# Performance work log

Measured on AMD Instinct MI355X. Metric: run time of the kernel, lower is better.

Reference implementation:

```python
import jax, jax.numpy as jnp
import numpy as np

B, N, D, H, F = 16, 257, 1024, 16, 4096
HD = D // H
EPS = 1e-5
GATING_TEMP = 0.25  # gating_hyperparam for steep_sigmoid
SCALE = HD ** -0.5


def layer_norm(x, g, b):
    mu = jnp.mean(x, axis=-1, keepdims=True)
    var = jnp.mean(jnp.square(x - mu), axis=-1, keepdims=True)
    return (x - mu) * jax.lax.rsqrt(var + EPS) * g + b


def quick_gelu(x):
    return x * jax.nn.sigmoid(1.702 * x)


def setup_inputs() -> dict:
    key = jax.random.key(0)
    ks = jax.random.split(key, 24)
    s = 0.02
    inp = {
        'hidden_states': jax.random.normal(ks[0], (B, N, D), jnp.float32),
        'cached_hidden': jax.random.normal(ks[1], (B, N, D), jnp.float32),
        'cached_q': jax.random.normal(ks[2], (B, N, D), jnp.float32),
        'cached_k': jax.random.normal(ks[3], (B, N, D), jnp.float32),
        'cached_v': jax.random.normal(ks[4], (B, N, D), jnp.float32),
        'ln1_g': jnp.ones((D,), jnp.float32),
        'ln1_b': jnp.zeros((D,), jnp.float32),
        'wq': jax.random.normal(ks[5], (D, D), jnp.float32) * s,
        'bq': jnp.zeros((D,), jnp.float32),
        'wk': jax.random.normal(ks[6], (D, D), jnp.float32) * s,
        'bk': jnp.zeros((D,), jnp.float32),
        'wv': jax.random.normal(ks[7], (D, D), jnp.float32) * s,
        'bv': jnp.zeros((D,), jnp.float32),
        'wo': jax.random.normal(ks[8], (D, D), jnp.float32) * s,
        'bo': jnp.zeros((D,), jnp.float32),
        'ln2_g': jnp.ones((D,), jnp.float32),
        'ln2_b': jnp.zeros((D,), jnp.float32),
        'w1': jax.random.normal(ks[9], (D, F), jnp.float32) * s,
        'b1': jnp.zeros((F,), jnp.float32),
        'w2': jax.random.normal(ks[10], (F, D), jnp.float32) * s,
        'b2': jnp.zeros((D,), jnp.float32),
        'threshold': jnp.float32(0.5),
    }
    return inp


def reference(hidden_states, cached_hidden, cached_q, cached_k, cached_v,
              ln1_g, ln1_b, wq, bq, wk, bk, wv, bv, wo, bo,
              ln2_g, ln2_b, w1, b1, w2, b2, threshold):
    # layer_norm1 + QKV projection (layer_norm1_qkv_projection)
    h_ln = layer_norm(hidden_states, ln1_g, ln1_b)
    q = h_ln @ wq + bq
    k = h_ln @ wk + bk
    v = h_ln @ wv + bv

    # reuse module: cosine^1 similarity vs cached hidden, steep_sigmoid gating
    # against learned threshold; soft gather/scatter blend of cached states.
    num = jnp.sum(cached_hidden * hidden_states, axis=-1)           # [B,N]
    den = (jnp.linalg.norm(cached_hidden, axis=-1)
           * jnp.linalg.norm(hidden_states, axis=-1) + 1e-8)
    sim = num / den                                                 # [B,N]
    gate = jax.nn.sigmoid((sim - threshold) / GATING_TEMP)[..., None]  # [B,N,1]

    hidden = gate * cached_hidden + (1.0 - gate) * hidden_states
    q = gate * cached_q + (1.0 - gate) * q
    k = gate * cached_k + (1.0 - gate) * k
    v = gate * cached_v + (1.0 - gate) * v

    # manual bmm-softmax-bmm attention
    qh = (q * SCALE).reshape(B, N, H, HD).transpose(0, 2, 1, 3)  # [B,H,N,hd]
    kh = k.reshape(B, N, H, HD).transpose(0, 2, 1, 3)
    vh = v.reshape(B, N, H, HD).transpose(0, 2, 1, 3)
    scores = jnp.einsum('bhqd,bhkd->bhqk', qh, kh)
    probs = jax.nn.softmax(scores, axis=-1)
    attn = jnp.einsum('bhqk,bhkd->bhqd', probs, vh)
    attn = attn.transpose(0, 2, 1, 3).reshape(B, N, D)
    attn = attn @ wo + bo

    hidden = hidden + attn
    residual = hidden
    hidden = layer_norm(hidden, ln2_g, ln2_b)
    hidden = quick_gelu(hidden @ w1 + b1) @ w2 + b2
    return residual + hidden
```

## Files before the change

kernel.cpp:

```cpp
#include <hip/hip_runtime.h>
#include <hip/hip_bf16.h>
#include <stdint.h>

#define BB   16
#define SEQ  257
#define DD   1024
#define NH   16
#define HD_  64
#define FF   4096
#define MM   (BB*SEQ)
#define MPAD2 4352
#define SPAD 272
#define VPAD 288
#define SCALE_Q 0.125f

typedef __bf16 bf16x8 __attribute__((ext_vector_type(8)));
typedef float  f32x4  __attribute__((ext_vector_type(4)));
typedef unsigned short u16;

__device__ __forceinline__ u16 f2bf(float f) {
  uint32_t u = __float_as_uint(f);
  uint32_t r = (u + 0x7FFFu + ((u >> 16) & 1u)) >> 16;
  return (u16)r;
}
__device__ __forceinline__ float bf2f(u16 u) {
  return __uint_as_float(((uint32_t)u) << 16);
}
__device__ __forceinline__ void gll16(const void* g, void* l) {
  __builtin_amdgcn_global_load_lds(
      (const __attribute__((address_space(1))) void*)g,
      (__attribute__((address_space(3))) void*)l, 16, 0, 0);
}
__device__ __forceinline__ float wsum(float v) {
  #pragma unroll
  for (int o = 1; o < 64; o <<= 1) v += __shfl_xor(v, o);
  return v;
}

__global__ __launch_bounds__(256) void transpose_all(
    const float* __restrict__ wq, const float* __restrict__ wk,
    const float* __restrict__ wv, const float* __restrict__ wo,
    const float* __restrict__ w1, const float* __restrict__ w2,
    u16* __restrict__ wqkvT, u16* __restrict__ woT,
    u16* __restrict__ w1T, u16* __restrict__ w2T) {
  __shared__ float tile[64][65];
  const int bid = blockIdx.x;
  const float* src;  u16* dst;  int R, C, b;
  if (bid < 768)       { int s = bid >> 8;  b = bid & 255;
                         src = s==0?wq:(s==1?wk:wv);  dst = wqkvT + s*1024*1024;
                         R = 1024; C = 1024; }
  else if (bid < 1024) { src = wo;  dst = woT;  b = bid - 768;   R = 1024; C = 1024; }
  else if (bid < 2048) { src = w1;  dst = w1T;  b = bid - 1024;  R = 1024; C = 4096; }
  else                 { src = w2;  dst = w2T;  b = bid - 2048;  R = 4096; C = 1024; }
  const int ctiles = C >> 6;
  const int r0 = (b / ctiles) << 6, c0 = (b % ctiles) << 6;
  const int tx = threadIdx.x & 63, ty = threadIdx.x >> 6;
  #pragma unroll
  for (int it = 0; it < 16; ++it) {
    int rr = it * 4 + ty;
    tile[rr][tx] = src[(size_t)(r0 + rr) * C + c0 + tx];
  }
  __syncthreads();
  #pragma unroll
  for (int it = 0; it < 16; ++it) {
    int rr = it * 4 + ty;
    dst[(size_t)(c0 + rr) * R + r0 + tx] = f2bf(tile[tx][rr]);
  }
}

__global__ __launch_bounds__(256) void vtrans_kernel(
    const u16* __restrict__ vb, u16* __restrict__ vt) {
  __shared__ u16 tile[64][72];
  const int bh = blockIdx.x, c = blockIdx.y;
  const int tx = threadIdx.x & 63, ty = threadIdx.x >> 6;
  const u16* src = vb + (size_t)bh * SPAD * HD_;
  u16* dst = vt + (size_t)bh * HD_ * VPAD;
  #pragma unroll
  for (int it = 0; it < 16; ++it) {
    int r = it * 4 + ty;
    int nn = c * 64 + r;  int nnc = nn < SPAD ? nn : SPAD - 1;
    tile[r][tx] = src[(size_t)nnc * HD_ + tx];
  }
  __syncthreads();
  #pragma unroll
  for (int it = 0; it < 16; ++it) {
    int hd = it * 4 + ty;
    int col = c * 64 + tx;
    if (col < VPAD) dst[(size_t)hd * VPAD + col] = tile[tx][hd];
  }
}

__global__ __launch_bounds__(256) void ln1_gate_kernel(
    const float* __restrict__ h, const float* __restrict__ c,
    const float* __restrict__ g, const float* __restrict__ bta,
    const float* __restrict__ thr, u16* __restrict__ hln,
    float* __restrict__ hblend, float* __restrict__ gate) {
  int m = blockIdx.x, t = threadIdx.x, l = t & 63, w = t >> 6;
  const float4 hv = *(const float4*)(h + (size_t)m * DD + t * 4);
  const float4 cv = *(const float4*)(c + (size_t)m * DD + t * 4);
  float sh = hv.x + hv.y + hv.z + hv.w;
  float sh2 = hv.x*hv.x + hv.y*hv.y + hv.z*hv.z + hv.w*hv.w;
  float sch = hv.x*cv.x + hv.y*cv.y + hv.z*cv.z + hv.w*cv.w;
  float sc2 = cv.x*cv.x + cv.y*cv.y + cv.z*cv.z + cv.w*cv.w;
  sh = wsum(sh); sh2 = wsum(sh2); sch = wsum(sch); sc2 = wsum(sc2);
  __shared__ float red[4][4];
  if (l == 0) { red[w][0]=sh; red[w][1]=sh2; red[w][2]=sch; red[w][3]=sc2; }
  __syncthreads();
  float Sh  = red[0][0]+red[1][0]+red[2][0]+red[3][0];
  float Sh2 = red[0][1]+red[1][1]+red[2][1]+red[3][1];
  float Sch = red[0][2]+red[1][2]+red[2][2]+red[3][2];
  float Sc2 = red[0][3]+red[1][3]+red[2][3]+red[3][3];
  float mean = Sh * (1.f/DD);
  float var  = Sh2 * (1.f/DD) - mean*mean;
  float rs   = rsqrtf(var + 1e-5f);
  float sim  = Sch / (sqrtf(Sc2)*sqrtf(Sh2) + 1e-8f);
  float gv   = 1.f / (1.f + __expf(-(sim - thr[0]) * 4.0f));
  float4 gg = *(const float4*)(g + t*4);
  float4 bb = *(const float4*)(bta + t*4);
  ushort4 ob;
  ob.x = f2bf((hv.x-mean)*rs*gg.x + bb.x);
  ob.y = f2bf((hv.y-mean)*rs*gg.y + bb.y);
  ob.z = f2bf((hv.z-mean)*rs*gg.z + bb.z);
  ob.w = f2bf((hv.w-mean)*rs*gg.w + bb.w);
  *(ushort4*)(hln + (size_t)m * DD + t * 4) = ob;
  float4 hb;
  hb.x = gv*cv.x + (1.f-gv)*hv.x;  hb.y = gv*cv.y + (1.f-gv)*hv.y;
  hb.z = gv*cv.z + (1.f-gv)*hv.z;  hb.w = gv*cv.w + (1.f-gv)*hv.w;
  *(float4*)(hblend + (size_t)m * DD + t * 4) = hb;
  if (t == 0) gate[m] = gv;
}

__global__ __launch_bounds__(256) void ln2_kernel(
    const float* __restrict__ in, const float* __restrict__ g,
    const float* __restrict__ bta, u16* __restrict__ outb) {
  int m = blockIdx.x, t = threadIdx.x, l = t & 63, w = t >> 6;
  const float4 hv = *(const float4*)(in + (size_t)m * DD + t * 4);
  float sh = hv.x + hv.y + hv.z + hv.w;
  float sh2 = hv.x*hv.x + hv.y*hv.y + hv.z*hv.z + hv.w*hv.w;
  sh = wsum(sh); sh2 = wsum(sh2);
  __shared__ float red[4][2];
  if (l == 0) { red[w][0] = sh; red[w][1] = sh2; }
  __syncthreads();
  float Sh  = red[0][0]+red[1][0]+red[2][0]+red[3][0];
  float Sh2 = red[0][1]+red[1][1]+red[2][1]+red[3][1];
  float mean = Sh * (1.f/DD);
  float rs = rsqrtf(Sh2 * (1.f/DD) - mean*mean + 1e-5f);
  float4 gg = *(const float4*)(g + t*4);
  float4 bb = *(const float4*)(bta + t*4);
  ushort4 ob;
  ob.x = f2bf((hv.x-mean)*rs*gg.x + bb.x);
  ob.y = f2bf((hv.y-mean)*rs*gg.y + bb.y);
  ob.z = f2bf((hv.z-mean)*rs*gg.z + bb.z);
  ob.w = f2bf((hv.w-mean)*rs*gg.w + bb.w);
  *(ushort4*)(outb + (size_t)m * DD + t * 4) = ob;
}

template<int EPI>
__global__ __launch_bounds__(256) void gemm_bt(
    const u16* __restrict__ A, const u16* __restrict__ Bt,
    int Kstride, int Kiter,
    const float* __restrict__ bias,
    const float* __restrict__ gate,
    const float* __restrict__ c0, const float* __restrict__ c1, const float* __restrict__ c2,
    const float* __restrict__ bq, const float* __restrict__ bk, const float* __restrict__ bv,
    u16* __restrict__ qb, u16* __restrict__ kb, u16* __restrict__ vb,
    const float* __restrict__ addsrc, float* __restrict__ outf,
    u16* __restrict__ outb, u16* __restrict__ partb) {
  const int tid = threadIdx.x, w = tid >> 6, l = tid & 63, lr = l & 15, lh = l >> 4;
  const int Mt = gridDim.x;
  const int f = blockIdx.y * Mt + blockIdx.x;
  const int nwg = Mt * gridDim.y;
  const int swz = (f & 7) * (nwg >> 3) + (f >> 3);
  const int m0 = (swz % Mt) * 128, n0 = (swz / Mt) * 128;
  const int kBase = blockIdx.z * Kiter;
  const int wm = w >> 1, wn = w & 1;
  __shared__ u16 sA[2][8192], sB[2][8192];
  f32x4 acc[4][4];
  f32x4 zero = {0.f, 0.f, 0.f, 0.f};
  #pragma unroll
  for (int i = 0; i < 4; ++i)
    #pragma unroll
    for (int j = 0; j < 4; ++j) acc[i][j] = zero;

  const int rS = tid >> 3;
  const int srcC = ((tid & 7) ^ (rS & 7)) * 8;
  const u16* gA = A  + (size_t)(m0 + rS) * Kstride + kBase + srcC;
  const u16* gB = Bt + (size_t)(n0 + rS) * Kstride + kBase + srcC;
  const size_t rStep = (size_t)32 * Kstride;

  const int rdA = (wm*64 + lr) * 64;
  const int rdB = (wn*64 + lr) * 64;
  const int cx0 = ((lh ^ (lr & 7)) & 7) * 8;

  #define STAGE(BUF_, T_) do { \
    const int _ko = (T_) * 64; \
    _Pragma("unroll") \
    for (int _j = 0; _j < 4; ++_j) { \
      gll16(gA + _ko + _j*rStep, &sA[BUF_][_j*2048] + tid*8); \
      gll16(gB + _ko + _j*rStep, &sB[BUF_][_j*2048] + tid*8); \
    } } while(0)

  const int nt = Kiter >> 6;
  STAGE(0, 0);
  for (int t = 0; t < nt; ++t) {
    const int cur = t & 1;
    __syncthreads();
    if (t + 1 < nt) STAGE(cur ^ 1, t + 1);
    #pragma unroll
    for (int ks = 0; ks < 2; ++ks) {
      const int co = cx0 ^ (ks * 32);
      bf16x8 af[4], bfr[4];
      #pragma unroll
      for (int mi = 0; mi < 4; ++mi)
        af[mi] = *(const bf16x8*)&sA[cur][rdA + mi*1024 + co];
      #pragma unroll
      for (int ni = 0; ni < 4; ++ni)
        bfr[ni] = *(const bf16x8*)&sB[cur][rdB + ni*1024 + co];
      #pragma unroll
      for (int mi = 0; mi < 4; ++mi)
        #pragma unroll
        for (int ni = 0; ni < 4; ++ni)
          acc[mi][ni] = __builtin_amdgcn_mfma_f32_16x16x32_bf16(af[mi], bfr[ni], acc[mi][ni], 0, 0, 0);
    }
  }
  #undef STAGE

  if constexpr (EPI == 0) {
    const int which = n0 >> 10;
    const float* cb = which==0 ? bq : (which==1 ? bk : bv);
    const float* cp = which==0 ? c0 : (which==1 ? c1 : c2);
    u16* dst = which==0 ? qb : (which==1 ? kb : vb);
    const float scl = which==0 ? SCALE_Q : 1.0f;
    #pragma unroll
    for (int mi = 0; mi < 4; ++mi) {
      #pragma unroll
      for (int r = 0; r < 4; ++r) {
        const int row = m0 + wm*64 + mi*16 + lh*4 + r;
        if (row < MM) {
          const float gv = gate[row];
          const int bidx = row / SEQ, nn = row - bidx * SEQ;
          #pragma unroll
          for (int ni = 0; ni < 4; ++ni) {
            const int col = n0 + wn*64 + ni*16 + lr;
            const int d = col & 1023, hd = d & 63, hh = d >> 6;
            const float lin = acc[mi][ni][r] + cb[d];
            const float val = (gv * cp[(size_t)row*DD + d] + (1.f - gv) * lin) * scl;
            dst[((size_t)(bidx*NH + hh)*SPAD + nn)*HD_ + hd] = f2bf(val);
          }
        }
      }
    }
  } else if constexpr (EPI == 1) {
    #pragma unroll
    for (int mi = 0; mi < 4; ++mi)
      #pragma unroll
      for (int r = 0; r < 4; ++r) {
        const int row = m0 + wm*64 + mi*16 + lh*4 + r;
        if (row < MM) {
          #pragma unroll
          for (int ni = 0; ni < 4; ++ni) {
            const int col = n0 + wn*64 + ni*16 + lr;
            outf[(size_t)row*DD + col] = acc[mi][ni][r] + bias[col] + addsrc[(size_t)row*DD + col];
          }
        }
      }
  } else if constexpr (EPI == 2) {
    #pragma unroll
    for (int mi = 0; mi < 4; ++mi)
      #pragma unroll
      for (int r = 0; r < 4; ++r) {
        const int row = m0 + wm*64 + mi*16 + lh*4 + r;
        if (row < MM) {
          #pragma unroll
          for (int ni = 0; ni < 4; ++ni) {
            const int col = n0 + wn*64 + ni*16 + lr;
            const float x = acc[mi][ni][r] + bias[col];
            const float s = 1.f / (1.f + __expf(-1.702f * x));
            outb[(size_t)row*FF + col] = f2bf(x * s);
          }
        }
      }
  } else {
    u16* pp = partb + (size_t)blockIdx.z * ((size_t)MPAD2 * 1024);
    #pragma unroll
    for (int mi = 0; mi < 4; ++mi)
      #pragma unroll
      for (int r = 0; r < 4; ++r) {
        const int row = m0 + wm*64 + mi*16 + lh*4 + r;
        if (row < MM) {
          #pragma unroll
          for (int ni = 0; ni < 4; ++ni) {
            const int col = n0 + wn*64 + ni*16 + lr;
            pp[(size_t)row*1024 + col] = f2bf(acc[mi][ni][r]);
          }
        }
      }
  }
}

__global__ __launch_bounds__(256) void reduce_mlp2(
    const u16* __restrict__ parts, const float* __restrict__ bias,
    const float* __restrict__ resid, float* __restrict__ out) {
  const size_t PS = (size_t)MPAD2 * 1024;
  const int row = blockIdx.x, t = threadIdx.x, c = t * 4;
  const size_t base = (size_t)row * 1024 + c;
  float4 r = *(const float4*)(resid + base);
  float4 b = *(const float4*)(bias + c);
  float o0 = r.x + b.x, o1 = r.y + b.y, o2 = r.z + b.z, o3 = r.w + b.w;
  #pragma unroll
  for (int p = 0; p < 2; ++p) {
    ushort4 u = *(const ushort4*)(parts + p*PS + base);
    o0 += bf2f(u.x);  o1 += bf2f(u.y);  o2 += bf2f(u.z);  o3 += bf2f(u.w);
  }
  float4 o;  o.x = o0;  o.y = o1;  o.z = o2;  o.w = o3;
  *(float4*)(out + base) = o;
}

__global__ __launch_bounds__(256) void attn_kernel(
    const u16* __restrict__ qb, const u16* __restrict__ kb,
    const u16* __restrict__ vt, u16* __restrict__ attn_out) {
  __shared__ u16 P[64 * 296];
  const int bh = blockIdx.x, b = bh >> 4, hh = bh & 15;
  const int q0 = blockIdx.y * 64;
  const int tid = threadIdx.x, w = tid >> 6, l = tid & 63, lr = l & 15, lh = l >> 4;
  const u16* qp = qb + (size_t)bh * SPAD * HD_;
  const u16* kp = kb + (size_t)bh * SPAD * HD_;
  const u16* vp = vt + (size_t)bh * HD_ * VPAD;

  const int qr = q0 + w*16 + lr;
  const int qrc = qr < 271 ? qr : 271;
  bf16x8 aq0 = *(const bf16x8*)(qp + (size_t)qrc*HD_ + lh*8);
  bf16x8 aq1 = *(const bf16x8*)(qp + (size_t)qrc*HD_ + 32 + lh*8);

  f32x4 st[18];
  f32x4 zero = {0.f,0.f,0.f,0.f};
  #pragma unroll
  for (int t = 0; t < 18; ++t) st[t] = zero;
  #pragma unroll
  for (int t = 0; t < 18; ++t) {
    int key = t*16 + lr;  int keyc = key < 271 ? key : 271;
    bf16x8 b0 = *(const bf16x8*)(kp + (size_t)keyc*HD_ + lh*8);
    bf16x8 b1 = *(const bf16x8*)(kp + (size_t)keyc*HD_ + 32 + lh*8);
    st[t] = __builtin_amdgcn_mfma_f32_16x16x32_bf16(aq0, b0, st[t], 0, 0, 0);
    st[t] = __builtin_amdgcn_mfma_f32_16x16x32_bf16(aq1, b1, st[t], 0, 0, 0);
  }
  #pragma unroll
  for (int t = 0; t < 18; ++t) {
    int key = t*16 + lr;
    if (key >= SEQ) { st[t][0]=-1e30f; st[t][1]=-1e30f; st[t][2]=-1e30f; st[t][3]=-1e30f; }
  }
  float mr[4], sr[4];
  #pragma unroll
  for (int r = 0; r < 4; ++r) {
    float m = st[0][r];
    #pragma unroll
    for (int t = 1; t < 18; ++t) m = fmaxf(m, st[t][r]);
    m = fmaxf(m, __shfl_xor(m, 1));  m = fmaxf(m, __shfl_xor(m, 2));
    m = fmaxf(m, __shfl_xor(m, 4));  m = fmaxf(m, __shfl_xor(m, 8));
    mr[r] = m;  sr[r] = 0.f;
  }
  #pragma unroll
  for (int t = 0; t < 18; ++t)
    #pragma unroll
    for (int r = 0; r < 4; ++r) {
      float p = __expf(st[t][r] - mr[r]);
      st[t][r] = p;  sr[r] += p;
    }
  #pragma unroll
  for (int r = 0; r < 4; ++r) {
    sr[r] += __shfl_xor(sr[r], 1);  sr[r] += __shfl_xor(sr[r], 2);
    sr[r] += __shfl_xor(sr[r], 4);  sr[r] += __shfl_xor(sr[r], 8);
  }
  #pragma unroll
  for (int t = 0; t < 18; ++t)
    #pragma unroll
    for (int r = 0; r < 4; ++r)
      P[(w*16 + lh*4 + r)*296 + t*16 + lr] = f2bf(st[t][r]);
  __syncthreads();

  f32x4 o[4];
  #pragma unroll
  for (int ni = 0; ni < 4; ++ni) o[ni] = zero;
  #pragma unroll
  for (int ks = 0; ks < 9; ++ks) {
    bf16x8 pa = *(const bf16x8*)&P[(w*16 + lr)*296 + ks*32 + lh*8];
    #pragma unroll
    for (int ni = 0; ni < 4; ++ni) {
      bf16x8 bv_ = *(const bf16x8*)(vp + (size_t)(ni*16 + lr)*VPAD + ks*32 + lh*8);
      o[ni] = __builtin_amdgcn_mfma_f32_16x16x32_bf16(pa, bv_, o[ni], 0, 0, 0);
    }
  }
  #pragma unroll
  for (int r = 0; r < 4; ++r) {
    const int qrow = q0 + w*16 + lh*4 + r;
    if (qrow < SEQ) {
      const float inv = 1.f / sr[r];
      #pragma unroll
      for (int ni = 0; ni < 4; ++ni)
        attn_out[(size_t)(b*SEQ + qrow)*DD + hh*HD_ + ni*16 + lr] = f2bf(o[ni][r] * inv);
    }
  }
}

extern "C" void kernel_launch(void* const* d_in, const int* in_sizes, int n_in,
                              void* d_out, int out_size, void* d_ws, size_t ws_size,
                              hipStream_t stream) {
  (void)in_sizes; (void)n_in; (void)out_size; (void)ws_size;
  const float* hidden   = (const float*)d_in[0];
  const float* cached_h = (const float*)d_in[1];
  const float* cached_q = (const float*)d_in[2];
  const float* cached_k = (const float*)d_in[3];
  const float* cached_v = (const float*)d_in[4];
  const float* ln1_g = (const float*)d_in[5];
  const float* ln1_b = (const float*)d_in[6];
  const float* wq = (const float*)d_in[7];
  const float* bq = (const float*)d_in[8];
  const float* wk = (const float*)d_in[9];
  const float* bk = (const float*)d_in[10];
  const float* wv = (const float*)d_in[11];
  const float* bv = (const float*)d_in[12];
  const float* wo = (const float*)d_in[13];
  const float* bo = (const float*)d_in[14];
  const float* ln2_g = (const float*)d_in[15];
  const float* ln2_b = (const float*)d_in[16];
  const float* w1 = (const float*)d_in[17];
  const float* b1 = (const float*)d_in[18];
  const float* w2 = (const float*)d_in[19];
  const float* b2 = (const float*)d_in[20];
  const float* thr = (const float*)d_in[21];
  float* out = (float*)d_out;

  char* ws = (char*)d_ws;
  size_t off = 0;
  auto alloc = [&](size_t bytes) {
    void* p = ws + off;  off += (bytes + 255) & ~(size_t)255;  return p;
  };
  u16*   wqkvT  = (u16*)alloc(3072ull * 1024 * 2);
  u16*   woT    = (u16*)alloc(1024ull * 1024 * 2);
  u16*   w1T    = (u16*)alloc(4096ull * 1024 * 2);
  u16*   w2T    = (u16*)alloc(1024ull * 4096 * 2);
  float* gate   = (float*)alloc((size_t)MPAD2 * 4);
  float* resid2 = (float*)alloc((size_t)MPAD2 * DD * 4);
  u16*   regA   = (u16*)alloc((size_t)MPAD2 * DD * 2);
  u16 *hln = regA, *attn_o = regA, *ln2out = regA;
  const size_t QKV_B  = (size_t)256 * SPAD * HD_ * 2;
  const size_t VT_B   = (size_t)256 * HD_ * VPAD * 2;
  const size_t PART_B = (size_t)MPAD2 * 1024 * 2;
  const size_t partsOff = 3*QKV_B + VT_B;
  char*  regB   = (char*)alloc(partsOff + 2*PART_B);
  u16*   qbuf   = (u16*)regB;
  u16*   kbuf   = (u16*)(regB + QKV_B);
  u16*   vbuf   = (u16*)(regB + 2*QKV_B);
  u16*   vtb    = (u16*)(regB + 3*QKV_B);
  float* hblend = (float*)(regB + partsOff);
  u16*   mid    = (u16*)regB;
  u16*   parts  = (u16*)(regB + partsOff);

  dim3 blk(256);
  transpose_all<<<dim3(3072), blk, 0, stream>>>(wq, wk, wv, wo, w1, w2,
                                                wqkvT, woT, w1T, w2T);

  ln1_gate_kernel<<<dim3(MM), blk, 0, stream>>>(hidden, cached_h, ln1_g, ln1_b, thr,
                                                hln, hblend, gate);

  gemm_bt<0><<<dim3(33, 24), blk, 0, stream>>>(hln, wqkvT, 1024, 1024, nullptr,
      gate, cached_q, cached_k, cached_v, bq, bk, bv, qbuf, kbuf, vbuf,
      nullptr, nullptr, nullptr, nullptr);

  vtrans_kernel<<<dim3(256, 5), blk, 0, stream>>>(vbuf, vtb);
  attn_kernel<<<dim3(256, 5), blk, 0, stream>>>(qbuf, kbuf, vtb, attn_o);

  gemm_bt<1><<<dim3(33, 8), blk, 0, stream>>>(attn_o, woT, 1024, 1024, bo,
      nullptr, nullptr, nullptr, nullptr, nullptr, nullptr, nullptr,
      nullptr, nullptr, nullptr, hblend, resid2, nullptr, nullptr);

  ln2_kernel<<<dim3(MM), blk, 0, stream>>>(resid2, ln2_g, ln2_b, ln2out);

  gemm_bt<2><<<dim3(33, 32), blk, 0, stream>>>(ln2out, w1T, 1024, 1024, b1,
      nullptr, nullptr, nullptr, nullptr, nullptr, nullptr, nullptr,
      nullptr, nullptr, nullptr, nullptr, nullptr, mid, nullptr);

  gemm_bt<3><<<dim3(33, 8, 2), blk, 0, stream>>>(mid, w2T, 4096, 2048, nullptr,
      nullptr, nullptr, nullptr, nullptr, nullptr, nullptr, nullptr,
      nullptr, nullptr, nullptr, nullptr, nullptr, nullptr, parts);

  reduce_mlp2<<<dim3(MM), blk, 0, stream>>>(parts, b2, resid2, out);
}
```

Before: 308.2 us.

## Widen GEMM tiles to 128x256 with BK=32 and fix XCD swizzle for uneven grids

Changes the shared bf16 GEMM from 128x128 tiles with a 64-wide K step to 128x256 tiles with a 32-wide K step. Each wave now holds 4x8 accumulators, and the LDS layout and swizzle are reworked for 32-element rows. The XCD block remap now handles grid sizes that are not a multiple of 8, and launch bounds request 2 blocks per CU. The aim is more MFMA work per LDS fragment load and fewer blocks per GEMM. The cost is double the accumulator registers, more sync points per K, and fewer blocks to fill the CUs on the smaller GEMMs.

Result: slower. 326.3 us (+5.9%).

```diff
diff --git a/kernel.cpp b/kernel.cpp
--- a/kernel.cpp
+++ b/kernel.cpp
@@ -156,7 +156,7 @@
 }
 
 template<int EPI>
-__global__ __launch_bounds__(256) void gemm_bt(
+__global__ __launch_bounds__(256, 2) void gemm_bt(
     const u16* __restrict__ A, const u16* __restrict__ Bt,
     int Kstride, int Kiter,
     const float* __restrict__ bias,
@@ -170,58 +170,59 @@
   const int Mt = gridDim.x;
   const int f = blockIdx.y * Mt + blockIdx.x;
   const int nwg = Mt * gridDim.y;
-  const int swz = (f & 7) * (nwg >> 3) + (f >> 3);
-  const int m0 = (swz % Mt) * 128, n0 = (swz / Mt) * 128;
+  const int q8 = nwg >> 3, r8 = nwg & 7, xcd = f & 7, lin = f >> 3;
+  const int swz = (xcd < r8 ? xcd * (q8 + 1) : r8 * (q8 + 1) + (xcd - r8) * q8) + lin;
+  const int m0 = (swz % Mt) * 128, n0 = (swz / Mt) * 256;
   const int kBase = blockIdx.z * Kiter;
   const int wm = w >> 1, wn = w & 1;
-  __shared__ u16 sA[2][8192], sB[2][8192];
-  f32x4 acc[4][4];
+  __shared__ u16 sA[2][4096];
+  __shared__ u16 sB[2][8192];
+  f32x4 acc[4][8];
   f32x4 zero = {0.f, 0.f, 0.f, 0.f};
   #pragma unroll
   for (int i = 0; i < 4; ++i)
     #pragma unroll
-    for (int j = 0; j < 4; ++j) acc[i][j] = zero;
-
-  const int rS = tid >> 3;
-  const int srcC = ((tid & 7) ^ (rS & 7)) * 8;
+    for (int j = 0; j < 8; ++j) acc[i][j] = zero;
+
+  const int rS = tid >> 2;
+  const int srcC = (((tid & 3) ^ ((tid >> 3) & 3)) * 8);
   const u16* gA = A  + (size_t)(m0 + rS) * Kstride + kBase + srcC;
   const u16* gB = Bt + (size_t)(n0 + rS) * Kstride + kBase + srcC;
-  const size_t rStep = (size_t)32 * Kstride;
-
-  const int rdA = (wm*64 + lr) * 64;
-  const int rdB = (wn*64 + lr) * 64;
-  const int cx0 = ((lh ^ (lr & 7)) & 7) * 8;
+  const size_t rStep = (size_t)64 * Kstride;
+
+  const int sL = (lr >> 1) & 3;
+  const int coff = ((lh ^ sL) & 3) * 8;
+  const int rdA = (wm*64  + lr) * 32 + coff;
+  const int rdB = (wn*128 + lr) * 32 + coff;
 
   #define STAGE(BUF_, T_) do { \
-    const int _ko = (T_) * 64; \
-    _Pragma("unroll") \
-    for (int _j = 0; _j < 4; ++_j) { \
-      gll16(gA + _ko + _j*rStep, &sA[BUF_][_j*2048] + tid*8); \
-      gll16(gB + _ko + _j*rStep, &sB[BUF_][_j*2048] + tid*8); \
-    } } while(0)
-
-  const int nt = Kiter >> 6;
+    const int _ko = (T_) << 5; \
+    gll16(gA + _ko,           &sA[BUF_][0]    + tid*8); \
+    gll16(gA + _ko + rStep,   &sA[BUF_][2048] + tid*8); \
+    gll16(gB + _ko,           &sB[BUF_][0]    + tid*8); \
+    gll16(gB + _ko + rStep,   &sB[BUF_][2048] + tid*8); \
+    gll16(gB + _ko + 2*rStep, &sB[BUF_][4096] + tid*8); \
+    gll16(gB + _ko + 3*rStep, &sB[BUF_][6144] + tid*8); \
+  } while(0)
+
+  const int nt = Kiter >> 5;
   STAGE(0, 0);
   for (int t = 0; t < nt; ++t) {
     const int cur = t & 1;
     __syncthreads();
     if (t + 1 < nt) STAGE(cur ^ 1, t + 1);
-    #pragma unroll
-    for (int ks = 0; ks < 2; ++ks) {
-      const int co = cx0 ^ (ks * 32);
-      bf16x8 af[4], bfr[4];
-      #pragma unroll
-      for (int mi = 0; mi < 4; ++mi)
-        af[mi] = *(const bf16x8*)&sA[cur][rdA + mi*1024 + co];
-      #pragma unroll
-      for (int ni = 0; ni < 4; ++ni)
-        bfr[ni] = *(const bf16x8*)&sB[cur][rdB + ni*1024 + co];
-      #pragma unroll
-      for (int mi = 0; mi < 4; ++mi)
-        #pragma unroll
-        for (int ni = 0; ni < 4; ++ni)
-          acc[mi][ni] = __builtin_amdgcn_mfma_f32_16x16x32_bf16(af[mi], bfr[ni], acc[mi][ni], 0, 0, 0);
-    }
+    bf16x8 af[4], bfr[8];
+    #pragma unroll
+    for (int mi = 0; mi < 4; ++mi)
+      af[mi] = *(const bf16x8*)&sA[cur][rdA + mi*512];
+    #pragma unroll
+    for (int ni = 0; ni < 8; ++ni)
+      bfr[ni] = *(const bf16x8*)&sB[cur][rdB + ni*512];
+    #pragma unroll
+    for (int mi = 0; mi < 4; ++mi)
+      #pragma unroll
+      for (int ni = 0; ni < 8; ++ni)
+        acc[mi][ni] = __builtin_amdgcn_mfma_f32_16x16x32_bf16(af[mi], bfr[ni], acc[mi][ni], 0, 0, 0);
   }
   #undef STAGE
 
@@ -240,11 +241,11 @@
           const float gv = gate[row];
           const int bidx = row / SEQ, nn = row - bidx * SEQ;
           #pragma unroll
-          for (int ni = 0; ni < 4; ++ni) {
-            const int col = n0 + wn*64 + ni*16 + lr;
+          for (int ni = 0; ni < 8; ++ni) {
+            const int col = n0 + wn*128 + ni*16 + lr;
             const int d = col & 1023, hd = d & 63, hh = d >> 6;
-            const float lin = acc[mi][ni][r] + cb[d];
-            const float val = (gv * cp[(size_t)row*DD + d] + (1.f - gv) * lin) * scl;
+            const float lin2 = acc[mi][ni][r] + cb[d];
+            const float val = (gv * cp[(size_t)row*DD + d] + (1.f - gv) * lin2) * scl;
             dst[((size_t)(bidx*NH + hh)*SPAD + nn)*HD_ + hd] = f2bf(val);
           }
         }
@@ -258,8 +259,8 @@
         const int row = m0 + wm*64 + mi*16 + lh*4 + r;
         if (row < MM) {
           #pragma unroll
-          for (int ni = 0; ni < 4; ++ni) {
-            const int col = n0 + wn*64 + ni*16 + lr;
+          for (int ni = 0; ni < 8; ++ni) {
+            const int col = n0 + wn*128 + ni*16 + lr;
             outf[(size_t)row*DD + col] = acc[mi][ni][r] + bias[col] + addsrc[(size_t)row*DD + col];
           }
         }
@@ -272,8 +273,8 @@
         const int row = m0 + wm*64 + mi*16 + lh*4 + r;
         if (row < MM) {
           #pragma unroll
-          for (int ni = 0; ni < 4; ++ni) {
-            const int col = n0 + wn*64 + ni*16 + lr;
+          for (int ni = 0; ni < 8; ++ni) {
+            const int col = n0 + wn*128 + ni*16 + lr;
             const float x = acc[mi][ni][r] + bias[col];
             const float s = 1.f / (1.f + __expf(-1.702f * x));
             outb[(size_t)row*FF + col] = f2bf(x * s);
@@ -289,8 +290,8 @@
         const int row = m0 + wm*64 + mi*16 + lh*4 + r;
         if (row < MM) {
           #pragma unroll
-          for (int ni = 0; ni < 4; ++ni) {
-            const int col = n0 + wn*64 + ni*16 + lr;
+          for (int ni = 0; ni < 8; ++ni) {
+            const int col = n0 + wn*128 + ni*16 + lr;
             pp[(size_t)row*1024 + col] = f2bf(acc[mi][ni][r]);
           }
         }
@@ -463,24 +464,24 @@
   ln1_gate_kernel<<<dim3(MM), blk, 0, stream>>>(hidden, cached_h, ln1_g, ln1_b, thr,
                                                 hln, hblend, gate);
 
-  gemm_bt<0><<<dim3(33, 24), blk, 0, stream>>>(hln, wqkvT, 1024, 1024, nullptr,
+  gemm_bt<0><<<dim3(33, 12), blk, 0, stream>>>(hln, wqkvT, 1024, 1024, nullptr,
       gate, cached_q, cached_k, cached_v, bq, bk, bv, qbuf, kbuf, vbuf,
       nullptr, nullptr, nullptr, nullptr);
 
   vtrans_kernel<<<dim3(256, 5), blk, 0, stream>>>(vbuf, vtb);
   attn_kernel<<<dim3(256, 5), blk, 0, stream>>>(qbuf, kbuf, vtb, attn_o);
 
-  gemm_bt<1><<<dim3(33, 8), blk, 0, stream>>>(attn_o, woT, 1024, 1024, bo,
+  gemm_bt<1><<<dim3(33, 4), blk, 0, stream>>>(attn_o, woT, 1024, 1024, bo,
       nullptr, nullptr, nullptr, nullptr, nullptr, nullptr, nullptr,
       nullptr, nullptr, nullptr, hblend, resid2, nullptr, nullptr);
 
   ln2_kernel<<<dim3(MM), blk, 0, stream>>>(resid2, ln2_g, ln2_b, ln2out);
 
-  gemm_bt<2><<<dim3(33, 32), blk, 0, stream>>>(ln2out, w1T, 1024, 1024, b1,
+  gemm_bt<2><<<dim3(33, 16), blk, 0, stream>>>(ln2out, w1T, 1024, 1024, b1,
       nullptr, nullptr, nullptr, nullptr, nullptr, nullptr, nullptr,
       nullptr, nullptr, nullptr, nullptr, nullptr, mid, nullptr);
 
-  gemm_bt<3><<<dim3(33, 8, 2), blk, 0, stream>>>(mid, w2T, 4096, 2048, nullptr,
+  gemm_bt<3><<<dim3(33, 4, 2), blk, 0, stream>>>(mid, w2T, 4096, 2048, nullptr,
       nullptr, nullptr, nullptr, nullptr, nullptr, nullptr, nullptr,
       nullptr, nullptr, nullptr, nullptr, nullptr, nullptr, parts);
 
```
